# Performance work log

Measured on AMD Instinct MI355X. Metric: run time of the kernel, lower is better.

Reference implementation:

```python
import jax, jax.numpy as jnp
import numpy as np


def setup_inputs() -> dict:
    key = jax.random.key(0)
    k1, k2, k3, k4 = jax.random.split(key, 4)
    in_features, out_features = 4096, 11008
    n_tokens = 64
    x = jax.random.normal(k1, (n_tokens, in_features), dtype=jnp.float32)
    # int8-valued weights stored as int32 (values in [-128, 127] range subset)
    weight_int = jax.random.randint(k2, (out_features, in_features), 0, 127, dtype=jnp.int32)
    weight_scale = jnp.float32(0.01)
    weight_zero_point = 3  # scalar int zero point
    bias = jax.random.normal(k3, (out_features,), dtype=jnp.float32) * 0.02
    return {
        "x": x,
        "weight_int": weight_int,
        "weight_scale": weight_scale,
        "weight_zero_point": weight_zero_point,
        "bias": bias,
    }


def reference(x, weight_int, weight_scale, weight_zero_point, bias):
    # Dequantize: W = (W_int - zp) * scale, shape [out, in]
    w = (weight_int.astype(jnp.float32) - jnp.float32(weight_zero_point)) * weight_scale
    # F.linear: y = x @ W^T + b
    out = jnp.einsum("ti,oi->to", x, w)
    return out + bias
```

## Files before the change

### kernel.cpp

```cpp
#include <hip/hip_runtime.h>
#include <hip/hip_bf16.h>

typedef __attribute__((ext_vector_type(8))) short short8;
typedef __attribute__((ext_vector_type(4))) float f32x4;
typedef __attribute__((ext_vector_type(4))) int   int4v;

#define IN_F   4096
#define OUT_F  11008
#define KSPLIT 4
#define KPART  (IN_F / KSPLIT)
#define BK     64
#define NIT    (KPART / BK)
#define DEPTH  3

__device__ __forceinline__ short bf16_rne(float f) {
    unsigned u = __builtin_bit_cast(unsigned, f);
    u += 0x7FFFu + ((u >> 16) & 1u);
    return (short)(u >> 16);
}

__device__ __forceinline__ void gld16(const void* g, void* l) {
    __builtin_amdgcn_global_load_lds(
        (const __attribute__((address_space(1))) unsigned int*)g,
        (__attribute__((address_space(3))) unsigned int*)l,
        16, 0, 0);
}

__device__ __forceinline__ short8 deq8(int4v q0, int4v q1, int zp) {
    short8 r;
#pragma unroll
    for (int j = 0; j < 4; ++j) {
        r[j]     = (short)(__builtin_bit_cast(unsigned, (float)(q0[j] - zp)) >> 16);
        r[j + 4] = (short)(__builtin_bit_cast(unsigned, (float)(q1[j] - zp)) >> 16);
    }
    return r;
}

__global__ __launch_bounds__(256)
void xcast(const float* __restrict__ x, unsigned short* __restrict__ xb) {
    const int i = (blockIdx.x * 256 + threadIdx.x) * 8;
    f32x4 a = *(const f32x4*)(x + i);
    f32x4 b = *(const f32x4*)(x + i + 4);
    short8 o;
#pragma unroll
    for (int j = 0; j < 4; ++j) { o[j] = bf16_rne(a[j]); o[j + 4] = bf16_rne(b[j]); }
    *(short8*)(xb + i) = o;
}

__global__ __launch_bounds__(256)
void binit(const float* __restrict__ bias, float* __restrict__ out) {
    const unsigned cid = blockIdx.x * 256 + threadIdx.x;
    const unsigned row = cid / (OUT_F / 8);
    const unsigned o   = (cid - row * (OUT_F / 8)) * 8;
    f32x4 b0 = *(const f32x4*)(bias + o);
    f32x4 b1 = *(const f32x4*)(bias + o + 4);
    float* dst = out + (size_t)row * OUT_F + o;
    *(f32x4*)dst = b0;
    *(f32x4*)(dst + 4) = b1;
}

#define STAGE(IT) do {                                                        \
    const int _s = (IT) % DEPTH;                                              \
    const int* _wsi = wsrc + (size_t)(IT) * BK;                               \
    gld16(_wsi,              (char*)wt[_s] + tid * 16);                       \
    gld16(_wsi + 16 * IN_F,  (char*)wt[_s] + 4096  + tid * 16);               \
    gld16(_wsi + 32 * IN_F,  (char*)wt[_s] + 8192  + tid * 16);               \
    gld16(_wsi + 48 * IN_F,  (char*)wt[_s] + 12288 + tid * 16);               \
    const unsigned short* _xsi = xsrc + (size_t)(IT) * BK;                    \
    gld16(_xsi,            (char*)xt[_s] + tid * 16);                         \
    gld16(_xsi + 32 * IN_F, (char*)xt[_s] + 4096 + tid * 16);                 \
} while (0)

#define COMPUTE(S) do {                                                       \
    const char* _wb = (const char*)wt[S] + wrow_off;                          \
    int4v _q00 = *(const int4v*)(_wb + cw00);                                 \
    int4v _q01 = *(const int4v*)(_wb + cw01);                                 \
    int4v _q10 = *(const int4v*)(_wb + cw10);                                 \
    int4v _q11 = *(const int4v*)(_wb + cw11);                                 \
    short8 _B0 = deq8(_q00, _q01, zp);                                        \
    short8 _B1 = deq8(_q10, _q11, zp);                                        \
    const char* _xb = (const char*)xt[S] + arow;                              \
    short8 _a;                                                                \
    _a = *(const short8*)(_xb +        ca0);                                  \
    acc0 = __builtin_amdgcn_mfma_f32_16x16x32_bf16(_a, _B0, acc0, 0, 0, 0);   \
    _a = *(const short8*)(_xb +        ca1);                                  \
    acc0 = __builtin_amdgcn_mfma_f32_16x16x32_bf16(_a, _B1, acc0, 0, 0, 0);   \
    _a = *(const short8*)(_xb + 2048 + ca0);                                  \
    acc1 = __builtin_amdgcn_mfma_f32_16x16x32_bf16(_a, _B0, acc1, 0, 0, 0);   \
    _a = *(const short8*)(_xb + 2048 + ca1);                                  \
    acc1 = __builtin_amdgcn_mfma_f32_16x16x32_bf16(_a, _B1, acc1, 0, 0, 0);   \
    _a = *(const short8*)(_xb + 4096 + ca0);                                  \
    acc2 = __builtin_amdgcn_mfma_f32_16x16x32_bf16(_a, _B0, acc2, 0, 0, 0);   \
    _a = *(const short8*)(_xb + 4096 + ca1);                                  \
    acc2 = __builtin_amdgcn_mfma_f32_16x16x32_bf16(_a, _B1, acc2, 0, 0, 0);   \
    _a = *(const short8*)(_xb + 6144 + ca0);                                  \
    acc3 = __builtin_amdgcn_mfma_f32_16x16x32_bf16(_a, _B0, acc3, 0, 0, 0);   \
    _a = *(const short8*)(_xb + 6144 + ca1);                                  \
    acc3 = __builtin_amdgcn_mfma_f32_16x16x32_bf16(_a, _B1, acc3, 0, 0, 0);   \
} while (0)

__global__ __launch_bounds__(256, 2)
void qlin6(const unsigned short* __restrict__ xb, const int* __restrict__ w,
           const float* __restrict__ scale_p, const int* __restrict__ zp_p,
           float* __restrict__ out)
{
    __shared__ __align__(16) int            wt[DEPTH][64 * BK];
    __shared__ __align__(16) unsigned short xt[DEPTH][64 * BK];

    const int tid  = threadIdx.x;
    const int lane = tid & 63;
    const int wv   = tid >> 6;
    const int l15  = lane & 15;
    const int lg   = lane >> 4;

    const int ob = blockIdx.x >> 2;
    const int kh = blockIdx.x & 3;
    const int o0 = ob * 64;
    const int kb = kh * KPART;

    const int   zp    = zp_p[0];
    const float scale = scale_p[0];

    const int wr = tid >> 4;
    const int wc = (tid & 15) ^ (wr & 7);
    const int* wsrc = w + (size_t)(o0 + wr) * IN_F + kb + wc * 4;

    const int xr = tid >> 3;
    const int xc = (tid & 7) ^ (xr & 7);
    const unsigned short* xsrc = xb + (size_t)xr * IN_F + kb + xc * 8;

    const int rswz = l15 & 7;
    const int wrow_off = (wv * 16 + l15) * 256;
    const int cw00 = ((lg * 2    ) ^ rswz) * 16;
    const int cw01 = ((lg * 2 + 1) ^ rswz) * 16;
    const int cw10 = ((8 + lg * 2    ) ^ rswz) * 16;
    const int cw11 = ((8 + lg * 2 + 1) ^ rswz) * 16;
    const int arow = l15 * 128;
    const int ca0  = ((lg    ) ^ rswz) * 16;
    const int ca1  = ((4 + lg) ^ rswz) * 16;

    f32x4 acc0 = {0.f, 0.f, 0.f, 0.f};
    f32x4 acc1 = {0.f, 0.f, 0.f, 0.f};
    f32x4 acc2 = {0.f, 0.f, 0.f, 0.f};
    f32x4 acc3 = {0.f, 0.f, 0.f, 0.f};

    STAGE(0);
    STAGE(1);

#pragma unroll 3
    for (int it = 0; it < NIT - 1; ++it) {
        asm volatile("s_waitcnt vmcnt(6)" ::: "memory");
        __builtin_amdgcn_s_barrier();
        if (it + 2 < NIT) STAGE(it + 2);
        COMPUTE(it % DEPTH);
    }
    asm volatile("s_waitcnt vmcnt(0)" ::: "memory");
    __builtin_amdgcn_s_barrier();
    COMPUTE((NIT - 1) % DEPTH);

    {
        const int o = o0 + wv * 16 + l15;
        float* op = out + o;
#pragma unroll
        for (int r = 0; r < 4; ++r) {
            const int tr = lg * 4 + r;
            unsafeAtomicAdd(op + (size_t)(tr     ) * OUT_F, scale * acc0[r]);
            unsafeAtomicAdd(op + (size_t)(tr + 16) * OUT_F, scale * acc1[r]);
            unsafeAtomicAdd(op + (size_t)(tr + 32) * OUT_F, scale * acc2[r]);
            unsafeAtomicAdd(op + (size_t)(tr + 48) * OUT_F, scale * acc3[r]);
        }
    }
}

extern "C" void kernel_launch(void* const* d_in, const int* in_sizes, int n_in,
                              void* d_out, int out_size, void* d_ws, size_t ws_size,
                              hipStream_t stream) {
    const float* x     = (const float*)d_in[0];
    const int*   w     = (const int*)d_in[1];
    const float* scale = (const float*)d_in[2];
    const int*   zp    = (const int*)d_in[3];
    const float* bias  = (const float*)d_in[4];
    float*       out   = (float*)d_out;
    unsigned short* xbf = (unsigned short*)d_ws;

    xcast<<<dim3(128), dim3(256), 0, stream>>>(x, xbf);
    binit<<<dim3(344), dim3(256), 0, stream>>>(bias, out);
    qlin6<<<dim3((OUT_F / 64) * KSPLIT), dim3(256), 0, stream>>>(xbf, w, scale, zp, out);
}
```

Measured before the change: 47.97 us.

## Load activations directly into registers, double K-split, fuse prep kernels

Activation tiles are no longer staged in LDS. Each lane now loads its bf16 fragments straight from global memory into registers, double-buffered between A and B register sets and issued one iteration ahead. The K split goes from 4 to 8 and occupancy is raised to 3 blocks per CU, and the x-cast and bias-init kernels are merged into a single launch. This is meant to cut LDS traffic and footprint, add parallelism, and remove one launch, at the cost of more register pressure and twice as many atomic adds to the output.

```diff
diff --git a/kernel.cpp b/kernel.cpp
--- a/kernel.cpp
+++ b/kernel.cpp
@@ -7,7 +7,7 @@
 
 #define IN_F   4096
 #define OUT_F  11008
-#define KSPLIT 4
+#define KSPLIT 8
 #define KPART  (IN_F / KSPLIT)
 #define BK     64
 #define NIT    (KPART / BK)
@@ -37,19 +37,18 @@
 }
 
 __global__ __launch_bounds__(256)
-void xcast(const float* __restrict__ x, unsigned short* __restrict__ xb) {
-    const int i = (blockIdx.x * 256 + threadIdx.x) * 8;
-    f32x4 a = *(const f32x4*)(x + i);
-    f32x4 b = *(const f32x4*)(x + i + 4);
-    short8 o;
+void prep(const float* __restrict__ x, const float* __restrict__ bias,
+          unsigned short* __restrict__ xb, float* __restrict__ out) {
+    const unsigned cid = blockIdx.x * 256 + threadIdx.x;
+    if (blockIdx.x < 128) {
+        const int i = cid * 8;
+        f32x4 a = *(const f32x4*)(x + i);
+        f32x4 b = *(const f32x4*)(x + i + 4);
+        short8 o;
 #pragma unroll
-    for (int j = 0; j < 4; ++j) { o[j] = bf16_rne(a[j]); o[j + 4] = bf16_rne(b[j]); }
-    *(short8*)(xb + i) = o;
-}
-
-__global__ __launch_bounds__(256)
-void binit(const float* __restrict__ bias, float* __restrict__ out) {
-    const unsigned cid = blockIdx.x * 256 + threadIdx.x;
+        for (int j = 0; j < 4; ++j) { o[j] = bf16_rne(a[j]); o[j + 4] = bf16_rne(b[j]); }
+        *(short8*)(xb + i) = o;
+    }
     const unsigned row = cid / (OUT_F / 8);
     const unsigned o   = (cid - row * (OUT_F / 8)) * 8;
     f32x4 b0 = *(const f32x4*)(bias + o);
@@ -59,53 +58,55 @@
     *(f32x4*)(dst + 4) = b1;
 }
 
-#define STAGE(IT) do {                                                        \
+#define STAGE_W(IT) do {                                                      \
     const int _s = (IT) % DEPTH;                                              \
     const int* _wsi = wsrc + (size_t)(IT) * BK;                               \
-    gld16(_wsi,              (char*)wt[_s] + tid * 16);                       \
-    gld16(_wsi + 16 * IN_F,  (char*)wt[_s] + 4096  + tid * 16);               \
-    gld16(_wsi + 32 * IN_F,  (char*)wt[_s] + 8192  + tid * 16);               \
-    gld16(_wsi + 48 * IN_F,  (char*)wt[_s] + 12288 + tid * 16);               \
-    const unsigned short* _xsi = xsrc + (size_t)(IT) * BK;                    \
-    gld16(_xsi,            (char*)xt[_s] + tid * 16);                         \
-    gld16(_xsi + 32 * IN_F, (char*)xt[_s] + 4096 + tid * 16);                 \
+    gld16(_wsi,             (char*)wt[_s] + tid * 16);                        \
+    gld16(_wsi + 16 * IN_F, (char*)wt[_s] + 4096  + tid * 16);                \
+    gld16(_wsi + 32 * IN_F, (char*)wt[_s] + 8192  + tid * 16);                \
+    gld16(_wsi + 48 * IN_F, (char*)wt[_s] + 12288 + tid * 16);                \
 } while (0)
 
-#define COMPUTE(S) do {                                                       \
-    const char* _wb = (const char*)wt[S] + wrow_off;                          \
+#define XLOAD(IT, S) do {                                                     \
+    const size_t _o = (size_t)(IT) * 128;                                     \
+    asm volatile("global_load_dwordx4 %0, %2, off\n\t"                        \
+                 "global_load_dwordx4 %1, %2, off offset:64"                  \
+        : "=&v"(xf##S##0a), "=&v"(xf##S##0b) : "v"(xq0 + _o) : "memory");     \
+    asm volatile("global_load_dwordx4 %0, %2, off\n\t"                        \
+                 "global_load_dwordx4 %1, %2, off offset:64"                  \
+        : "=&v"(xf##S##1a), "=&v"(xf##S##1b) : "v"(xq1 + _o) : "memory");     \
+    asm volatile("global_load_dwordx4 %0, %2, off\n\t"                        \
+                 "global_load_dwordx4 %1, %2, off offset:64"                  \
+        : "=&v"(xf##S##2a), "=&v"(xf##S##2b) : "v"(xq2 + _o) : "memory");     \
+    asm volatile("global_load_dwordx4 %0, %2, off\n\t"                        \
+                 "global_load_dwordx4 %1, %2, off offset:64"                  \
+        : "=&v"(xf##S##3a), "=&v"(xf##S##3b) : "v"(xq3 + _o) : "memory");     \
+} while (0)
+
+#define COMPUTE(SL, S) do {                                                   \
+    const char* _wb = (const char*)wt[SL] + wrow_off;                         \
     int4v _q00 = *(const int4v*)(_wb + cw00);                                 \
     int4v _q01 = *(const int4v*)(_wb + cw01);                                 \
     int4v _q10 = *(const int4v*)(_wb + cw10);                                 \
     int4v _q11 = *(const int4v*)(_wb + cw11);                                 \
     short8 _B0 = deq8(_q00, _q01, zp);                                        \
     short8 _B1 = deq8(_q10, _q11, zp);                                        \
-    const char* _xb = (const char*)xt[S] + arow;                              \
-    short8 _a;                                                                \
-    _a = *(const short8*)(_xb +        ca0);                                  \
-    acc0 = __builtin_amdgcn_mfma_f32_16x16x32_bf16(_a, _B0, acc0, 0, 0, 0);   \
-    _a = *(const short8*)(_xb +        ca1);                                  \
-    acc0 = __builtin_amdgcn_mfma_f32_16x16x32_bf16(_a, _B1, acc0, 0, 0, 0);   \
-    _a = *(const short8*)(_xb + 2048 + ca0);                                  \
-    acc1 = __builtin_amdgcn_mfma_f32_16x16x32_bf16(_a, _B0, acc1, 0, 0, 0);   \
-    _a = *(const short8*)(_xb + 2048 + ca1);                                  \
-    acc1 = __builtin_amdgcn_mfma_f32_16x16x32_bf16(_a, _B1, acc1, 0, 0, 0);   \
-    _a = *(const short8*)(_xb + 4096 + ca0);                                  \
-    acc2 = __builtin_amdgcn_mfma_f32_16x16x32_bf16(_a, _B0, acc2, 0, 0, 0);   \
-    _a = *(const short8*)(_xb + 4096 + ca1);                                  \
-    acc2 = __builtin_amdgcn_mfma_f32_16x16x32_bf16(_a, _B1, acc2, 0, 0, 0);   \
-    _a = *(const short8*)(_xb + 6144 + ca0);                                  \
-    acc3 = __builtin_amdgcn_mfma_f32_16x16x32_bf16(_a, _B0, acc3, 0, 0, 0);   \
-    _a = *(const short8*)(_xb + 6144 + ca1);                                  \
-    acc3 = __builtin_amdgcn_mfma_f32_16x16x32_bf16(_a, _B1, acc3, 0, 0, 0);   \
+    acc0 = __builtin_amdgcn_mfma_f32_16x16x32_bf16(xf##S##0a, _B0, acc0, 0, 0, 0); \
+    acc0 = __builtin_amdgcn_mfma_f32_16x16x32_bf16(xf##S##0b, _B1, acc0, 0, 0, 0); \
+    acc1 = __builtin_amdgcn_mfma_f32_16x16x32_bf16(xf##S##1a, _B0, acc1, 0, 0, 0); \
+    acc1 = __builtin_amdgcn_mfma_f32_16x16x32_bf16(xf##S##1b, _B1, acc1, 0, 0, 0); \
+    acc2 = __builtin_amdgcn_mfma_f32_16x16x32_bf16(xf##S##2a, _B0, acc2, 0, 0, 0); \
+    acc2 = __builtin_amdgcn_mfma_f32_16x16x32_bf16(xf##S##2b, _B1, acc2, 0, 0, 0); \
+    acc3 = __builtin_amdgcn_mfma_f32_16x16x32_bf16(xf##S##3a, _B0, acc3, 0, 0, 0); \
+    acc3 = __builtin_amdgcn_mfma_f32_16x16x32_bf16(xf##S##3b, _B1, acc3, 0, 0, 0); \
 } while (0)
 
-__global__ __launch_bounds__(256, 2)
-void qlin6(const unsigned short* __restrict__ xb, const int* __restrict__ w,
+__global__ __launch_bounds__(256, 3)
+void qlin7(const unsigned short* __restrict__ xb, const int* __restrict__ w,
            const float* __restrict__ scale_p, const int* __restrict__ zp_p,
            float* __restrict__ out)
 {
-    __shared__ __align__(16) int            wt[DEPTH][64 * BK];
-    __shared__ __align__(16) unsigned short xt[DEPTH][64 * BK];
+    __shared__ __align__(16) int wt[DEPTH][64 * BK];
 
     const int tid  = threadIdx.x;
     const int lane = tid & 63;
@@ -113,8 +114,8 @@
     const int l15  = lane & 15;
     const int lg   = lane >> 4;
 
-    const int ob = blockIdx.x >> 2;
-    const int kh = blockIdx.x & 3;
+    const int ob = blockIdx.x >> 3;
+    const int kh = blockIdx.x & 7;
     const int o0 = ob * 64;
     const int kb = kh * KPART;
 
@@ -125,9 +126,10 @@
     const int wc = (tid & 15) ^ (wr & 7);
     const int* wsrc = w + (size_t)(o0 + wr) * IN_F + kb + wc * 4;
 
-    const int xr = tid >> 3;
-    const int xc = (tid & 7) ^ (xr & 7);
-    const unsigned short* xsrc = xb + (size_t)xr * IN_F + kb + xc * 8;
+    const char* xq0 = (const char*)(xb + (size_t)(0 * 16 + l15) * IN_F + kb + lg * 8);
+    const char* xq1 = (const char*)(xb + (size_t)(1 * 16 + l15) * IN_F + kb + lg * 8);
+    const char* xq2 = (const char*)(xb + (size_t)(2 * 16 + l15) * IN_F + kb + lg * 8);
+    const char* xq3 = (const char*)(xb + (size_t)(3 * 16 + l15) * IN_F + kb + lg * 8);
 
     const int rswz = l15 & 7;
     const int wrow_off = (wv * 16 + l15) * 256;
@@ -135,28 +137,33 @@
     const int cw01 = ((lg * 2 + 1) ^ rswz) * 16;
     const int cw10 = ((8 + lg * 2    ) ^ rswz) * 16;
     const int cw11 = ((8 + lg * 2 + 1) ^ rswz) * 16;
-    const int arow = l15 * 128;
-    const int ca0  = ((lg    ) ^ rswz) * 16;
-    const int ca1  = ((4 + lg) ^ rswz) * 16;
 
     f32x4 acc0 = {0.f, 0.f, 0.f, 0.f};
     f32x4 acc1 = {0.f, 0.f, 0.f, 0.f};
     f32x4 acc2 = {0.f, 0.f, 0.f, 0.f};
     f32x4 acc3 = {0.f, 0.f, 0.f, 0.f};
 
-    STAGE(0);
-    STAGE(1);
+    short8 xfA0a, xfA0b, xfA1a, xfA1b, xfA2a, xfA2b, xfA3a, xfA3b;
+    short8 xfB0a, xfB0b, xfB1a, xfB1b, xfB2a, xfB2b, xfB3a, xfB3b;
 
-#pragma unroll 3
-    for (int it = 0; it < NIT - 1; ++it) {
-        asm volatile("s_waitcnt vmcnt(6)" ::: "memory");
+    STAGE_W(0);
+    XLOAD(0, A);
+    STAGE_W(1);
+
+#pragma unroll
+    for (int it = 0; it < NIT; ++it) {
+        if (it < NIT - 1) asm volatile("s_waitcnt vmcnt(4)" ::: "memory");
+        else              asm volatile("s_waitcnt vmcnt(0)" ::: "memory");
         __builtin_amdgcn_s_barrier();
-        if (it + 2 < NIT) STAGE(it + 2);
-        COMPUTE(it % DEPTH);
+        __builtin_amdgcn_sched_barrier(0);
+        if (it + 1 < NIT) {
+            if ((it + 1) & 1) XLOAD(it + 1, B);
+            else              XLOAD(it + 1, A);
+        }
+        if (it + 2 < NIT) STAGE_W(it + 2);
+        if (it & 1) COMPUTE(it % DEPTH, B);
+        else        COMPUTE(it % DEPTH, A);
     }
-    asm volatile("s_waitcnt vmcnt(0)" ::: "memory");
-    __builtin_amdgcn_s_barrier();
-    COMPUTE((NIT - 1) % DEPTH);
 
     {
         const int o = o0 + wv * 16 + l15;
@@ -183,7 +190,6 @@
     float*       out   = (float*)d_out;
     unsigned short* xbf = (unsigned short*)d_ws;
 
-    xcast<<<dim3(128), dim3(256), 0, stream>>>(x, xbf);
-    binit<<<dim3(344), dim3(256), 0, stream>>>(bias, out);
-    qlin6<<<dim3((OUT_F / 64) * KSPLIT), dim3(256), 0, stream>>>(xbf, w, scale, zp, out);
+    prep<<<dim3(344), dim3(256), 0, stream>>>(x, bias, xbf, out);
+    qlin7<<<dim3((OUT_F / 64) * KSPLIT), dim3(256), 0, stream>>>(xbf, w, scale, zp, out);
 }
```

Result: slower. 69.57 us (+45.0%).
